# Optimization experiments

Measured on AMD Instinct MI355X. Metric: run time of the kernel, lower is better.

## Reference

```python
import jax, jax.numpy as jnp
import numpy as np

EPS = 1e-12
NUM_KNOTS = 30


def _pchip_slopes(y, x):
    """Shape-preserving PCHIP slopes at knots. y,x: [K], K>2, x strictly increasing."""
    h = x[1:] - x[:-1]                      # [K-1]
    delta = (y[1:] - y[:-1]) / (h + EPS)    # [K-1]
    hkm1, hk = h[:-1], h[1:]
    w1 = 2.0 * hk + hkm1
    w2 = hk + 2.0 * hkm1
    same_sign = delta[:-1] * delta[1:] > 0
    d_int = (w1 + w2) / (w1 / (delta[:-1] + EPS) + w2 / (delta[1:] + EPS))
    d_mid = jnp.where(same_sign, d_int, jnp.zeros_like(d_int))  # [K-2]
    # one-sided endpoint slopes with monotonicity limiting
    d0 = ((2.0 * h[0] + h[1]) * delta[0] - h[0] * delta[1]) / (h[0] + h[1] + EPS)
    dN = ((2.0 * h[-1] + h[-2]) * delta[-1] - h[-1] * delta[-2]) / (h[-1] + h[-2] + EPS)

    def _limit(di, de):
        di = jnp.where(di * de <= 0, jnp.zeros_like(di), di)
        return jnp.where(jnp.abs(di) > 3.0 * jnp.abs(de), 3.0 * de, di)

    d0 = _limit(d0, delta[0])
    dN = _limit(dN, delta[-1])
    return jnp.concatenate([d0[None], d_mid, dN[None]])  # [K]


def setup_inputs() -> dict:
    key = jax.random.key(0)
    k1, k2 = jax.random.split(key)
    x = jax.random.uniform(k1, (8192, 4096), dtype=jnp.float32)  # inputs inside knot domain [0,1)
    knots = jnp.linspace(0.0, 1.0, NUM_KNOTS, dtype=jnp.float32)  # buffer: uniform knots
    coeffs = jax.random.normal(k2, (NUM_KNOTS,), dtype=jnp.float32) * 0.5  # learned knot values
    return {"x": x, "knots": knots, "coeffs": coeffs}


def reference(x, knots, coeffs):
    """PCHIP cubic Hermite spline evaluated elementwise at x."""
    K = knots.shape[0]
    d = _pchip_slopes(coeffs, knots)
    xc = jnp.clip(x, knots[0], knots[-1])
    idx = jnp.clip(jnp.searchsorted(knots, xc) - 1, 0, K - 2)
    xk, xk1 = knots[idx], knots[idx + 1]
    yk, yk1 = coeffs[idx], coeffs[idx + 1]
    dk, dk1 = d[idx], d[idx + 1]
    h = xk1 - xk
    safe_h = jnp.where(jnp.abs(h) < EPS, jnp.ones_like(h), h)
    t = jnp.where(jnp.abs(h) < EPS, jnp.zeros_like(xc), (xc - xk) / safe_h)
    t2 = t * t
    t3 = t2 * t
    h00 = 2.0 * t3 - 3.0 * t2 + 1.0
    h10 = t3 - 2.0 * t2 + t
    h01 = -2.0 * t3 + 3.0 * t2
    h11 = t3 - t2
    return h00 * yk + h10 * safe_h * dk + h01 * yk1 + h11 * safe_h * dk1
```

## Files before the change

kernel.cpp:

```cpp
#include <hip/hip_runtime.h>

#define EPSF 1e-12f
#define NKNOTS 30
#define NINT 29

typedef float fvec4 __attribute__((ext_vector_type(4)));


__global__ __launch_bounds__(256) void SimpleSpline_kernel(
    const float* __restrict__ x,
    const float* __restrict__ knots,
    const float* __restrict__ coeffs,
    float* __restrict__ out,
    int n)
{
    __shared__ float a0[NINT], a1[NINT], a2[NINT], a3[NINT];
    __shared__ float dsh[NKNOTS];

    const int tid = threadIdx.x;

    if (tid < NKNOTS) {
        float d;
        if (tid == 0) {
            float h0 = knots[1] - knots[0];
            float h1 = knots[2] - knots[1];
            float de0 = (coeffs[1] - coeffs[0]) / (h0 + EPSF);
            float de1 = (coeffs[2] - coeffs[1]) / (h1 + EPSF);
            d = ((2.0f * h0 + h1) * de0 - h0 * de1) / (h0 + h1 + EPSF);
            if (d * de0 <= 0.0f) d = 0.0f;
            if (fabsf(d) > 3.0f * fabsf(de0)) d = 3.0f * de0;
        } else if (tid == NKNOTS - 1) {
            float hN = knots[NKNOTS - 1] - knots[NKNOTS - 2];
            float hM = knots[NKNOTS - 2] - knots[NKNOTS - 3];
            float deN = (coeffs[NKNOTS - 1] - coeffs[NKNOTS - 2]) / (hN + EPSF);
            float deM = (coeffs[NKNOTS - 2] - coeffs[NKNOTS - 3]) / (hM + EPSF);
            d = ((2.0f * hN + hM) * deN - hN * deM) / (hN + hM + EPSF);
            if (d * deN <= 0.0f) d = 0.0f;
            if (fabsf(d) > 3.0f * fabsf(deN)) d = 3.0f * deN;
        } else {
            float hkm1 = knots[tid] - knots[tid - 1];
            float hk   = knots[tid + 1] - knots[tid];
            float dkm1 = (coeffs[tid] - coeffs[tid - 1]) / (hkm1 + EPSF);
            float dk   = (coeffs[tid + 1] - coeffs[tid]) / (hk + EPSF);
            float w1 = 2.0f * hk + hkm1;
            float w2 = hk + 2.0f * hkm1;
            d = 0.0f;
            if (dkm1 * dk > 0.0f)
                d = (w1 + w2) / (w1 / (dkm1 + EPSF) + w2 / (dk + EPSF));
        }
        dsh[tid] = d;
    }
    __syncthreads();

    if (tid < NINT) {
        float h = knots[tid + 1] - knots[tid];
        float safe_h = (fabsf(h) < EPSF) ? 1.0f : h;
        float yk  = coeffs[tid];
        float yk1 = coeffs[tid + 1];
        float sdk  = safe_h * dsh[tid];
        float sdk1 = safe_h * dsh[tid + 1];
        a0[tid] = yk;
        a1[tid] = sdk;
        a2[tid] = 3.0f * (yk1 - yk) - 2.0f * sdk - sdk1;
        a3[tid] = 2.0f * (yk - yk1) + sdk + sdk1;
    }
    __syncthreads();

    auto eval1 = [&](float xc) -> float {
        xc = fminf(fmaxf(xc, 0.0f), 1.0f);
        float s = xc * 29.0f;
        int idx = (int)s;
        idx = idx > (NINT - 1) ? (NINT - 1) : idx;
        float t = s - (float)idx;
        float c0 = a0[idx], c1 = a1[idx], c2 = a2[idx], c3 = a3[idx];
        return fmaf(t, fmaf(t, fmaf(t, c3, c2), c1), c0);
    };

    auto eval4 = [&](fvec4 v) -> fvec4 {
        fvec4 r;
        r.x = eval1(v.x);
        r.y = eval1(v.y);
        r.z = eval1(v.z);
        r.w = eval1(v.w);
        return r;
    };

    const int n4 = n >> 2;
    const fvec4* __restrict__ xv = (const fvec4*)x;
    fvec4* __restrict__ ov = (fvec4*)out;

    const int gs = gridDim.x * blockDim.x;
    int i = blockIdx.x * blockDim.x + tid;

    for (; i + 3 * gs < n4; i += 4 * gs) {
        fvec4 v0 = xv[i];
        fvec4 v1 = xv[i + gs];
        fvec4 v2 = xv[i + 2 * gs];
        fvec4 v3 = xv[i + 3 * gs];
        fvec4 r0 = eval4(v0);
        fvec4 r1 = eval4(v1);
        fvec4 r2 = eval4(v2);
        fvec4 r3 = eval4(v3);
        __builtin_nontemporal_store(r0, &ov[i]);
        __builtin_nontemporal_store(r1, &ov[i + gs]);
        __builtin_nontemporal_store(r2, &ov[i + 2 * gs]);
        __builtin_nontemporal_store(r3, &ov[i + 3 * gs]);
    }
    for (; i < n4; i += gs) {
        __builtin_nontemporal_store(eval4(xv[i]), &ov[i]);
    }

    const int rem = n & 3;
    if (rem) {
        const int base = n4 << 2;
        const int gi = blockIdx.x * blockDim.x + tid;
        if (gi < rem) out[base + gi] = eval1(x[base + gi]);
    }
}

extern "C" void kernel_launch(void* const* d_in, const int* in_sizes, int n_in,
                              void* d_out, int out_size, void* d_ws, size_t ws_size,
                              hipStream_t stream) {
    const float* x      = (const float*)d_in[0];
    const float* knots  = (const float*)d_in[1];
    const float* coeffs = (const float*)d_in[2];
    float* out = (float*)d_out;
    const int n = in_sizes[0];

    const int block = 256;
    int n4 = n >> 2;
    int blocks = (n4 + block - 1) / block;
    if (blocks > 4096) blocks = 4096;
    if (blocks < 1) blocks = 1;

    SimpleSpline_kernel<<<blocks, block, 0, stream>>>(x, knots, coeffs, out, n);
}
```

Before: 244.1 us.

## Replace grid-stride loop with one-vec4-per-thread launch and plain stores

Removes the 4096-block cap and the unrolled grid-stride loop, so each thread handles exactly one float4 across a grid of about 32K blocks. Nontemporal stores become normal stores, and the clamp is moved after the multiply by 29. Every block now recomputes the PCHIP slopes and polynomial table in shared memory, and the two barriers run once per block instead of being amortized over many elements. It also loses the per-thread memory-level parallelism the 4x unrolling provided.

New measurement: 230.2 us. -5.7%, faster.

```diff
diff --git a/kernel.cpp b/kernel.cpp
--- a/kernel.cpp
+++ b/kernel.cpp
@@ -66,9 +66,8 @@
     }
     __syncthreads();
 
-    auto eval1 = [&](float xc) -> float {
-        xc = fminf(fmaxf(xc, 0.0f), 1.0f);
-        float s = xc * 29.0f;
+    auto eval1 = [&](float xi) -> float {
+        float s = fminf(fmaxf(xi * 29.0f, 0.0f), 29.0f);
         int idx = (int)s;
         idx = idx > (NINT - 1) ? (NINT - 1) : idx;
         float t = s - (float)idx;
@@ -76,44 +75,24 @@
         return fmaf(t, fmaf(t, fmaf(t, c3, c2), c1), c0);
     };
 
-    auto eval4 = [&](fvec4 v) -> fvec4 {
+    const int n4 = n >> 2;
+    const int gi = blockIdx.x * blockDim.x + tid;
+
+    if (gi < n4) {
+        const fvec4* __restrict__ xv = (const fvec4*)x;
+        fvec4* __restrict__ ov = (fvec4*)out;
+        fvec4 v = xv[gi];
         fvec4 r;
         r.x = eval1(v.x);
         r.y = eval1(v.y);
         r.z = eval1(v.z);
         r.w = eval1(v.w);
-        return r;
-    };
-
-    const int n4 = n >> 2;
-    const fvec4* __restrict__ xv = (const fvec4*)x;
-    fvec4* __restrict__ ov = (fvec4*)out;
-
-    const int gs = gridDim.x * blockDim.x;
-    int i = blockIdx.x * blockDim.x + tid;
-
-    for (; i + 3 * gs < n4; i += 4 * gs) {
-        fvec4 v0 = xv[i];
-        fvec4 v1 = xv[i + gs];
-        fvec4 v2 = xv[i + 2 * gs];
-        fvec4 v3 = xv[i + 3 * gs];
-        fvec4 r0 = eval4(v0);
-        fvec4 r1 = eval4(v1);
-        fvec4 r2 = eval4(v2);
-        fvec4 r3 = eval4(v3);
-        __builtin_nontemporal_store(r0, &ov[i]);
-        __builtin_nontemporal_store(r1, &ov[i + gs]);
-        __builtin_nontemporal_store(r2, &ov[i + 2 * gs]);
-        __builtin_nontemporal_store(r3, &ov[i + 3 * gs]);
-    }
-    for (; i < n4; i += gs) {
-        __builtin_nontemporal_store(eval4(xv[i]), &ov[i]);
+        ov[gi] = r;
     }
 
     const int rem = n & 3;
     if (rem) {
         const int base = n4 << 2;
-        const int gi = blockIdx.x * blockDim.x + tid;
         if (gi < rem) out[base + gi] = eval1(x[base + gi]);
     }
 }
@@ -130,7 +109,6 @@
     const int block = 256;
     int n4 = n >> 2;
     int blocks = (n4 + block - 1) / block;
-    if (blocks > 4096) blocks = 4096;
     if (blocks < 1) blocks = 1;
 
     SimpleSpline_kernel<<<blocks, block, 0, stream>>>(x, knots, coeffs, out, n);
```
